# Kernel tuning notes

Measured on AMD Instinct MI355X. Metric: run time of the kernel, lower is better.

## Reference

```python
import jax, jax.numpy as jnp
import numpy as np

N = 50000       # nodes
E = 800000      # edges (avg degree 16)
IN_DIM = 64
H = 64          # hidden_dim
OUT_DIM = 64
R = 8           # n_relations
L = 3           # n_layers
LN_EPS = 1e-5
NEG_SLOPE = 0.2


def _layer_norm(x, g, b):
    mu = jnp.mean(x, axis=-1, keepdims=True)
    var = jnp.mean((x - mu) ** 2, axis=-1, keepdims=True)
    return (x - mu) * jax.lax.rsqrt(var + LN_EPS) * g + b


def setup_inputs() -> dict:
    key = jax.random.key(0)
    ks = jax.random.split(key, 10)
    s = 0.05
    return {
        "x": jax.random.normal(ks[0], (N, IN_DIM), jnp.float32),
        "edge_index": jax.random.randint(ks[1], (2, E), 0, N),
        "edge_type": jax.random.randint(ks[2], (E,), 0, R),
        "W_in": jax.random.normal(ks[3], (H, IN_DIM), jnp.float32) * s,
        "b_in": jnp.zeros((H,), jnp.float32),
        "W_rel": jax.random.normal(ks[4], (R, H, H), jnp.float32) * s,   # no bias
        "W_gate": jax.random.normal(ks[5], (R, H, H), jnp.float32) * s,
        "b_gate": jnp.zeros((R, H), jnp.float32),
        "W_att": jax.random.normal(ks[6], (R, 2 * H), jnp.float32) * s,  # Linear(2H,1) per relation
        "b_att": jnp.zeros((R,), jnp.float32),
        "ln_gamma": jnp.ones((L, H), jnp.float32),
        "ln_beta": jnp.zeros((L, H), jnp.float32),
        "W_out": jax.random.normal(ks[7], (OUT_DIM, H), jnp.float32) * s,
        "b_out": jnp.zeros((OUT_DIM,), jnp.float32),
    }


def reference(x, edge_index, edge_type, W_in, b_in, W_rel, W_gate, b_gate,
              W_att, b_att, ln_gamma, ln_beta, W_out, b_out):
    src, dst = edge_index[0], edge_index[1]
    Wa_src, Wa_dst = W_att[:, :H], W_att[:, H:]      # [R,H] each
    seg = dst * R + edge_type                        # combined (node, relation) scatter key
    eidx = jnp.arange(E)

    h = jax.nn.relu(x @ W_in.T + b_in)               # [N,H]

    for layer in range(L):
        h_src = h[src]                               # [E,H] gather
        h_dst = h[dst]                               # [E,H] gather
        # attention score of each edge under its own relation's Linear(2H,1)
        scores_all = h_src @ Wa_src.T + h_dst @ Wa_dst.T + b_att   # [E,R]
        scores = scores_all[eidx, edge_type]                        # [E]
        scores = jax.nn.leaky_relu(scores, NEG_SLOPE)
        # softmax over dim=0 within each relation's edge set (as in the torch code)
        m = jax.ops.segment_max(scores, edge_type, num_segments=R)
        ex = jnp.exp(scores - m[edge_type])
        denom = jax.ops.segment_sum(ex, edge_type, num_segments=R)
        att = ex / denom[edge_type]                                 # [E]
        # relation-specific linear of source features (linear commutes with gather)
        hWr = jnp.einsum('nh,rkh->nrk', h, W_rel)                   # [N,R,H]
        msg = hWr[src, edge_type] * att[:, None]                    # [E,H]
        # per-relation scatter-add into destinations
        agg = jax.ops.segment_sum(msg, seg, num_segments=N * R)     # [N*R,H]
        agg = agg.reshape(N, R, H)
        gate = jax.nn.sigmoid(jnp.einsum('nh,rkh->nrk', h, W_gate) + b_gate)  # [N,R,H]
        h_new = jnp.mean(gate * agg, axis=1)         # sum(messages)/n_relations
        h = jax.nn.relu(_layer_norm(h + h_new, ln_gamma[layer], ln_beta[layer]))

    return h @ W_out.T + b_out
```

## Files before the change

kernel.cpp:

```cpp
#include <hip/hip_runtime.h>
#include <math.h>

#define NN 50000
#define EE 800000
#define HH 64
#define RR 8
#define LL 3
#define NR (NN * RR)
#define NB ((NR + 255) / 256)
#define LN_EPS 1e-5f
#define NEG_SLOPE 0.2f
#define LDH 68
#define OTB (16 * LDH)
#define DSPREAD 64

typedef __attribute__((ext_vector_type(8))) short bf8;
typedef __attribute__((ext_vector_type(4))) float f4;
typedef __attribute__((ext_vector_type(2))) float f2;
typedef __attribute__((ext_vector_type(8))) unsigned short us8;
typedef __attribute__((ext_vector_type(2))) unsigned int u2;
typedef __attribute__((ext_vector_type(4))) unsigned int u4;

#define PIN(x) asm volatile("" :: "v"(x))

__device__ __forceinline__ unsigned short bf16r(float f) {
    unsigned u = __float_as_uint(f);
    unsigned r = u + 0x7fffu + ((u >> 16) & 1u);
    return (unsigned short)(r >> 16);
}
__device__ __forceinline__ float bf2f(unsigned short u) {
    return __uint_as_float(((unsigned)u) << 16);
}
__device__ __forceinline__ void stage16(const void* g, void* l) {
    __builtin_amdgcn_global_load_lds(
        (const __attribute__((address_space(1))) void*)g,
        (__attribute__((address_space(3))) void*)l, 16, 0, 0);
}

__global__ __launch_bounds__(256) void proj_in(
    const float* __restrict__ x, const float* __restrict__ W,
    const float* __restrict__ bias, const unsigned short* __restrict__ WaB,
    float* __restrict__ h, unsigned short* __restrict__ hbf,
    float* __restrict__ s_src, float* __restrict__ s_dst) {
    __shared__ float WT[64 * LDH];
    __shared__ float xs[16 * LDH];
    __shared__ float hs[16 * LDH];
    int tid = threadIdx.x;
    int n0 = blockIdx.x * 16;
    #pragma unroll
    for (int s = 0; s < 16; ++s) {
        int idx = tid + 256 * s;
        int k = idx >> 6, i = idx & 63;
        WT[i * LDH + k] = W[idx];
    }
    int row = tid >> 4, cg = tid & 15;
    {
        f4 v = ((const f4*)x)[(size_t)(n0 + row) * 16 + cg];
        *(f4*)&xs[row * LDH + cg * 4] = v;
    }
    __syncthreads();
    f4 acc;
    {
        f4 b = *(const f4*)(bias + cg * 4);
        acc = b;
        #pragma unroll
        for (int i = 0; i < 64; ++i) {
            float xv = xs[row * LDH + i];
            f4 wt = *(const f4*)&WT[i * LDH + cg * 4];
            acc[0] += xv * wt[0];
            acc[1] += xv * wt[1];
            acc[2] += xv * wt[2];
            acc[3] += xv * wt[3];
        }
        #pragma unroll
        for (int j = 0; j < 4; ++j) acc[j] = fmaxf(acc[j], 0.f);
        int n = n0 + row;
        *(f4*)(h + (size_t)n * 64 + cg * 4) = acc;
        u2 u;
        u[0] = (unsigned)bf16r(acc[0]) | ((unsigned)bf16r(acc[1]) << 16);
        u[1] = (unsigned)bf16r(acc[2]) | ((unsigned)bf16r(acc[3]) << 16);
        *(u2*)(hbf + (size_t)n * 64 + cg * 4) = u;
        *(f4*)&hs[row * LDH + cg * 4] = acc;
    }
    __syncthreads();
    if (tid < 64) {
        int lane = tid;
        int quad = lane >> 4, lr = lane & 15;
        f4 sc = (f4){0.f, 0.f, 0.f, 0.f};
        #pragma unroll
        for (int kb = 0; kb < 2; ++kb) {
            const float* p = &hs[lr * LDH + kb * 32 + quad * 8];
            bf8 a;
            #pragma unroll
            for (int j = 0; j < 8; ++j) a[j] = (short)bf16r(p[j]);
            const bf8* bw = (const bf8*)(WaB + lr * 64 + kb * 32 + quad * 8);
            sc = __builtin_amdgcn_mfma_f32_16x16x32_bf16(a, *bw, sc, 0, 0, 0);
        }
        #pragma unroll
        for (int j = 0; j < 4; ++j) {
            int n = n0 + quad * 4 + j;
            if (lr < 8) s_src[n * 8 + lr] = sc[j];
            else        s_dst[n * 8 + (lr - 8)] = sc[j];
        }
    }
}

__global__ void edge_count(const int* __restrict__ ei, const int* __restrict__ et,
                           int* __restrict__ counts, int* __restrict__ rank) {
    int e = blockIdx.x * 256 + threadIdx.x;
    int d = ei[EE + e], t = et[e];
    rank[e] = atomicAdd(&counts[d * 8 + t], 1);
}

__global__ void scan1(const int* __restrict__ counts, int* __restrict__ offs,
                      int* __restrict__ bsum) {
    __shared__ int s[256];
    int tid = threadIdx.x;
    int i = blockIdx.x * 256 + tid;
    int v = (i < NR) ? counts[i] : 0;
    s[tid] = v; __syncthreads();
    for (int d = 1; d < 256; d <<= 1) {
        int x = (tid >= d) ? s[tid - d] : 0;
        __syncthreads();
        s[tid] += x;
        __syncthreads();
    }
    if (i < NR) offs[i] = s[tid] - v;
    if (tid == 255) bsum[blockIdx.x] = s[255];
}

__global__ void scan2(int* __restrict__ bsum) {
    __shared__ int s[1024];
    int tid = threadIdx.x;
    int carry = 0;
    for (int c0 = 0; c0 < NB; c0 += 1024) {
        int i = c0 + tid;
        int v = (i < NB) ? bsum[i] : 0;
        s[tid] = v; __syncthreads();
        for (int d = 1; d < 1024; d <<= 1) {
            int x = (tid >= d) ? s[tid - d] : 0;
            __syncthreads();
            s[tid] += x;
            __syncthreads();
        }
        if (i < NB) bsum[i] = carry + s[tid] - v;
        int tot = s[1023];
        __syncthreads();
        carry += tot;
    }
}

__global__ void edge_fill(const int* __restrict__ ei, const int* __restrict__ et,
                          const int* __restrict__ rank, const int* __restrict__ offs,
                          const int* __restrict__ bsum, u2* __restrict__ spack) {
    int e = blockIdx.x * 256 + threadIdx.x;
    int s = ei[e], d = ei[EE + e], t = et[e];
    int seg = d * 8 + t;
    int slot = offs[seg] + bsum[seg >> 8] + rank[e];
    spack[slot] = (u2){(unsigned)s, (unsigned)seg};
}

__global__ void cvt_w(const float* __restrict__ Wr, const float* __restrict__ Wg,
                      const float* __restrict__ Wa, const float* __restrict__ Wo,
                      unsigned short* __restrict__ WrB, unsigned short* __restrict__ WgB,
                      unsigned short* __restrict__ WaB, unsigned short* __restrict__ WoB) {
    int i = blockIdx.x * 256 + threadIdx.x;
    WrB[i] = bf16r(Wr[i]);
    WgB[i] = bf16r(Wg[i]);
    if (i < 1024) {
        int row = i >> 6, k = i & 63;
        float v = (row < 8) ? Wa[row * 128 + k] : Wa[(row - 8) * 128 + 64 + k];
        WaB[i] = bf16r(v);
    }
    if (i < 4096) WoB[i] = bf16r(Wo[i]);
}

__global__ void edge_softmax2(const u2* __restrict__ spack,
                              const float* __restrict__ s_src, const float* __restrict__ s_dst,
                              const float* __restrict__ b_att,
                              u2* __restrict__ epack, float* __restrict__ dpart) {
    __shared__ float lsum[4][8];
    int tid = threadIdx.x;
    if (tid < 32) lsum[tid >> 3][tid & 7] = 0.f;
    __syncthreads();
    int slot = blockIdx.x * 256 + tid;
    u2 sp = spack[slot];
    int src = (int)sp[0];
    int seg = (int)sp[1];
    int t = seg & 7;
    float sc = s_src[src * 8 + t] + s_dst[seg] + b_att[t];
    sc = (sc >= 0.f) ? sc : NEG_SLOPE * sc;
    float ex = __expf(sc);
    epack[slot] = (u2){(unsigned)src, __float_as_uint(ex)};
    atomicAdd(&lsum[tid >> 6][t], ex);
    __syncthreads();
    if (tid < 8) {
        float v = lsum[0][tid] + lsum[1][tid] + lsum[2][tid] + lsum[3][tid];
        atomicAdd(&dpart[(blockIdx.x & (DSPREAD - 1)) * 16 + tid], v);
    }
}

__global__ void denom_reduce(const float* __restrict__ dpartL,
                             float* __restrict__ idn8L) {
    __shared__ float sb[256];
    int t = threadIdx.x;
    int rb = t >> 3, ty = t & 7;
    float v = dpartL[rb * 16 + ty] + dpartL[(rb + 32) * 16 + ty];
    sb[t] = v; __syncthreads();
    for (int st = 128; st >= 8; st >>= 1) {
        if (t < st) sb[t] += sb[t + st];
        __syncthreads();
    }
    if (t < 8) idn8L[t] = 1.f / sb[t];
}

__global__ __launch_bounds__(256, 4) void gather_seg(
    const int* __restrict__ offs, const int* __restrict__ bsum,
    const u2* __restrict__ epack, const float* __restrict__ idn8L,
    const unsigned short* __restrict__ hbf_in,
    unsigned short* __restrict__ psG) {
    int tid = threadIdx.x;
    int segl = tid >> 1, half = tid & 1;
    int sidx = blockIdx.x * 128 + segl;
    int lo = offs[sidx] + bsum[sidx >> 8];
    int nxt = sidx + 1;
    int hi = (nxt < NR) ? (offs[nxt] + bsum[nxt >> 8]) : EE;
    int r = segl & 7, gn = segl >> 3;

    f4 d0 = *(const f4*)(idn8L);
    f4 d1 = *(const f4*)(idn8L + 4);
    float i01 = (r & 1) ? d0[1] : d0[0];
    float i23 = (r & 1) ? d0[3] : d0[2];
    float i45 = (r & 1) ? d1[1] : d1[0];
    float i67 = (r & 1) ? d1[3] : d1[2];
    float i03 = (r & 2) ? i23 : i01;
    float i47 = (r & 2) ? i67 : i45;
    float idn = (r & 4) ? i47 : i03;

    f2 acc[16];
    #pragma unroll
    for (int i = 0; i < 16; ++i) acc[i] = (f2){0.f, 0.f};

    for (int s = lo; s < hi; s += 4) {
        int i1 = (s + 1 < hi) ? s + 1 : s;
        int i2 = (s + 2 < hi) ? s + 2 : s;
        int i3 = (s + 3 < hi) ? s + 3 : s;
        u2 pk0 = epack[s], pk1 = epack[i1], pk2 = epack[i2], pk3 = epack[i3];
        float a0 = __uint_as_float(pk0[1]);
        float a1 = (s + 1 < hi) ? __uint_as_float(pk1[1]) : 0.f;
        float a2 = (s + 2 < hi) ? __uint_as_float(pk2[1]) : 0.f;
        float a3 = (s + 3 < hi) ? __uint_as_float(pk3[1]) : 0.f;
        const u4* hp0 = (const u4*)(hbf_in + ((size_t)(int)pk0[0] << 6) + half * 32);
        const u4* hp1 = (const u4*)(hbf_in + ((size_t)(int)pk1[0] << 6) + half * 32);
        const u4* hp2 = (const u4*)(hbf_in + ((size_t)(int)pk2[0] << 6) + half * 32);
        const u4* hp3 = (const u4*)(hbf_in + ((size_t)(int)pk3[0] << 6) + half * 32);
        #pragma unroll
        for (int q = 0; q < 4; ++q) {
            u4 v0 = hp0[q], v1 = hp1[q], v2 = hp2[q], v3 = hp3[q];
            #pragma unroll
            for (int k = 0; k < 4; ++k) {
                f2 w0, w1, w2, w3;
                w0[0] = __uint_as_float(v0[k] << 16);
                w0[1] = __uint_as_float(v0[k] & 0xffff0000u);
                w1[0] = __uint_as_float(v1[k] << 16);
                w1[1] = __uint_as_float(v1[k] & 0xffff0000u);
                w2[0] = __uint_as_float(v2[k] << 16);
                w2[1] = __uint_as_float(v2[k] & 0xffff0000u);
                w3[0] = __uint_as_float(v3[k] << 16);
                w3[1] = __uint_as_float(v3[k] & 0xffff0000u);
                acc[q * 4 + k] += (f2){a0, a0} * w0;
                acc[q * 4 + k] += (f2){a1, a1} * w1;
                acc[q * 4 + k] += (f2){a2, a2} * w2;
                acc[q * 4 + k] += (f2){a3, a3} * w3;
            }
        }
    }

    unsigned short* base = psG + ((size_t)blockIdx.x << 13) + gn * 512 + r * 64;
    #pragma unroll
    for (int q = 0; q < 4; ++q) {
        us8 o;
        #pragma unroll
        for (int k = 0; k < 4; ++k) {
            o[2 * k]     = bf16r(acc[q * 4 + k][0] * idn);
            o[2 * k + 1] = bf16r(acc[q * 4 + k][1] * idn);
        }
        int c2 = (half * 4 + q) ^ (gn & 7);
        *(us8*)(base + c2 * 8) = o;
    }
}

template<bool EMIT, bool OUT>
__global__ __launch_bounds__(256, 2) void combine_dense(
    const float* __restrict__ hbuf, const unsigned short* __restrict__ psG,
    const unsigned short* __restrict__ WrB, const unsigned short* __restrict__ WgB,
    const unsigned short* __restrict__ WaB, const unsigned short* __restrict__ WoB,
    const float* __restrict__ b_gate, const float* __restrict__ gamma,
    const float* __restrict__ beta, float* __restrict__ hout,
    unsigned short* __restrict__ hbf_out, float* __restrict__ ssrc_out,
    float* __restrict__ sdst_out, float* __restrict__ outp,
    const float* __restrict__ b_out) {
    __shared__ unsigned short psL[8192];
    __shared__ float hsL[1024];
    __shared__ float tf[32 * LDH];
    int tid = threadIdx.x;
    int n0 = blockIdx.x * 16;
    int w = tid >> 6, lane = tid & 63;
    int quad = lane >> 4, lr = lane & 15;
    int tn = w;

    {
        const char* pslice = (const char*)psG + ((size_t)blockIdx.x << 14);
        #pragma unroll
        for (int i = 0; i < 4; ++i) {
            unsigned off = i * 4096 + w * 1024;
            stage16(pslice + off + lane * 16, (char*)psL + off);
        }
        unsigned a = w * 1024 + lane * 16;
        unsigned sa = a ^ (((a >> 8) & 7u) << 4);
        stage16((const char*)(hbuf + (size_t)n0 * 64) + sa, (char*)hsL + a);
    }

    bf8 wfr[8][2], wfg[8][2];
    #pragma unroll
    for (int r = 0; r < 8; ++r) {
        #pragma unroll
        for (int kb = 0; kb < 2; ++kb) {
            wfr[r][kb] = *(const bf8*)(WrB + r * 4096 + (tn * 16 + lr) * 64 + kb * 32 + quad * 8);
            wfg[r][kb] = *(const bf8*)(WgB + r * 4096 + (tn * 16 + lr) * 64 + kb * 32 + quad * 8);
        }
    }
    float bgv[8];
    #pragma unroll
    for (int r = 0; r < 8; ++r) bgv[r] = b_gate[r * 64 + tn * 16 + lr];
    f4 gmv = *(const f4*)(gamma + (tid & 15) * 4);
    f4 btv = *(const f4*)(beta + (tid & 15) * 4);
    bf8 wa0, wa1, wo0, wo1;
    float bo = 0.f;
    if (EMIT) {
        wa0 = *(const bf8*)(WaB + lr * 64 + 0 * 32 + quad * 8);
        wa1 = *(const bf8*)(WaB + lr * 64 + 1 * 32 + quad * 8);
    }
    if (OUT) {
        wo0 = *(const bf8*)(WoB + (tn * 16 + lr) * 64 + 0 * 32 + quad * 8);
        wo1 = *(const bf8*)(WoB + (tn * 16 + lr) * 64 + 1 * 32 + quad * 8);
        bo = b_out[tn * 16 + lr];
    }
    #pragma unroll
    for (int r = 0; r < 8; ++r) {
        PIN(wfr[r][0]); PIN(wfr[r][1]);
        PIN(wfg[r][0]); PIN(wfg[r][1]);
        PIN(bgv[r]);
    }
    PIN(gmv); PIN(btv);
    if (EMIT) { PIN(wa0); PIN(wa1); }
    if (OUT)  { PIN(wo0); PIN(wo1); PIN(bo); }

    __syncthreads();

    bf8 a_h[2];
    #pragma unroll
    for (int kb = 0; kb < 2; ++kb) {
        unsigned c0 = (unsigned)(kb * 8 + quad * 2)     ^ (unsigned)(lr & 7);
        unsigned c1 = (unsigned)(kb * 8 + quad * 2 + 1) ^ (unsigned)(lr & 7);
        f4 p0 = *(const f4*)((const char*)hsL + lr * 256 + c0 * 16);
        f4 p1 = *(const f4*)((const char*)hsL + lr * 256 + c1 * 16);
        bf8 a;
        #pragma unroll
        for (int j = 0; j < 4; ++j) a[j] = (short)bf16r(p0[j]);
        #pragma unroll
        for (int j = 0; j < 4; ++j) a[4 + j] = (short)bf16r(p1[j]);
        a_h[kb] = a;
    }

    f4 acc = (f4){0.f, 0.f, 0.f, 0.f};
    #pragma unroll
    for (int r = 0; r < 8; ++r) {
        bf8 a_p[2];
        #pragma unroll
        for (int kb = 0; kb < 2; ++kb) {
            unsigned c = (unsigned)(kb * 4 + quad) ^ (unsigned)(lr & 7);
            a_p[kb] = *(const bf8*)((const char*)psL + lr * 1024 + r * 128 + c * 16);
        }
        f4 aggc = (f4){0.f, 0.f, 0.f, 0.f};
        f4 gacc = (f4){0.f, 0.f, 0.f, 0.f};
        #pragma unroll
        for (int kb = 0; kb < 2; ++kb) {
            aggc = __builtin_amdgcn_mfma_f32_16x16x32_bf16(a_p[kb], wfr[r][kb], aggc, 0, 0, 0);
            gacc = __builtin_amdgcn_mfma_f32_16x16x32_bf16(a_h[kb], wfg[r][kb], gacc, 0, 0, 0);
        }
        #pragma unroll
        for (int j = 0; j < 4; ++j) {
            float g = 1.f / (1.f + __expf(-(gacc[j] + bgv[r])));
            acc[j] += g * aggc[j];
        }
    }

    #pragma unroll
    for (int j = 0; j < 4; ++j) {
        int row = quad * 4 + j;
        int col = tn * 16 + lr;
        unsigned y = (unsigned)(row * 256 + col * 4);
        float hres = *(const float*)((const char*)hsL + (y ^ (((unsigned)(row & 7)) << 4)));
        tf[row * LDH + col] = hres + acc[j] * 0.125f;
    }
    __syncthreads();

    {
        int row = tid >> 4, c = tid & 15;
        int n = n0 + row;
        f4 tv = *(const f4*)&tf[row * LDH + c * 4];
        float s1 = tv[0] + tv[1] + tv[2] + tv[3];
        float s2 = tv[0]*tv[0] + tv[1]*tv[1] + tv[2]*tv[2] + tv[3]*tv[3];
        #pragma unroll
        for (int off = 1; off <= 8; off <<= 1) {
            s1 += __shfl_xor(s1, off, 64);
            s2 += __shfl_xor(s2, off, 64);
        }
        float mu = s1 * (1.f / 64.f);
        float var = s2 * (1.f / 64.f) - mu * mu;
        float rs = rsqrtf(var + LN_EPS);
        f4 ov;
        #pragma unroll
        for (int j = 0; j < 4; ++j)
            ov[j] = fmaxf((tv[j] - mu) * rs * gmv[j] + btv[j], 0.f);
        if (!OUT)
            *(f4*)(hout + (size_t)n * 64 + c * 4) = ov;
        *(f4*)&tf[OTB + row * LDH + c * 4] = ov;
        if (EMIT) {
            u2 u;
            u[0] = (unsigned)bf16r(ov[0]) | ((unsigned)bf16r(ov[1]) << 16);
            u[1] = (unsigned)bf16r(ov[2]) | ((unsigned)bf16r(ov[3]) << 16);
            *(u2*)(hbf_out + (size_t)n * 64 + c * 4) = u;
        }
    }

    if (EMIT) {
        __syncthreads();
        if (w == 0) {
            f4 sc = (f4){0.f, 0.f, 0.f, 0.f};
            #pragma unroll
            for (int kb = 0; kb < 2; ++kb) {
                const float* p = &tf[OTB + lr * LDH + kb * 32 + quad * 8];
                bf8 a;
                #pragma unroll
                for (int j = 0; j < 8; ++j) a[j] = (short)bf16r(p[j]);
                sc = __builtin_amdgcn_mfma_f32_16x16x32_bf16(a, kb ? wa1 : wa0, sc, 0, 0, 0);
            }
            #pragma unroll
            for (int j = 0; j < 4; ++j) {
                int n = n0 + quad * 4 + j;
                if (lr < 8) ssrc_out[n * 8 + lr] = sc[j];
                else        sdst_out[n * 8 + (lr - 8)] = sc[j];
            }
        }
    }

    if (OUT) {
        __syncthreads();
        f4 oc = (f4){0.f, 0.f, 0.f, 0.f};
        #pragma unroll
        for (int kb = 0; kb < 2; ++kb) {
            const float* p = &tf[OTB + lr * LDH + kb * 32 + quad * 8];
            bf8 a;
            #pragma unroll
            for (int j = 0; j < 8; ++j) a[j] = (short)bf16r(p[j]);
            oc = __builtin_amdgcn_mfma_f32_16x16x32_bf16(a, kb ? wo1 : wo0, oc, 0, 0, 0);
        }
        #pragma unroll
        for (int j = 0; j < 4; ++j)
            outp[(size_t)(n0 + quad * 4 + j) * 64 + tn * 16 + lr] = oc[j] + bo;
    }
}

extern "C" void kernel_launch(void* const* d_in, const int* in_sizes, int n_in,
                              void* d_out, int out_size, void* d_ws, size_t ws_size,
                              hipStream_t stream) {
    const float* x      = (const float*)d_in[0];
    const int*   ei     = (const int*)d_in[1];
    const int*   et     = (const int*)d_in[2];
    const float* W_in   = (const float*)d_in[3];
    const float* b_in   = (const float*)d_in[4];
    const float* W_rel  = (const float*)d_in[5];
    const float* W_gate = (const float*)d_in[6];
    const float* b_gate = (const float*)d_in[7];
    const float* W_att  = (const float*)d_in[8];
    const float* b_att  = (const float*)d_in[9];
    const float* ln_g   = (const float*)d_in[10];
    const float* ln_b   = (const float*)d_in[11];
    const float* W_out  = (const float*)d_in[12];
    const float* b_out  = (const float*)d_in[13];
    float* out = (float*)d_out;

    float* h0 = (float*)d_out;

    char* ws = (char*)d_ws;
    float* h1 = (float*)ws;                     ws += (size_t)NN * 64 * 4;
    unsigned short* hbfA = (unsigned short*)ws; ws += (size_t)NN * 64 * 2;
    unsigned short* hbfB = (unsigned short*)ws; ws += (size_t)NN * 64 * 2;
    float* s_src = (float*)ws;                  ws += (size_t)NN * 8 * 4;
    float* s_dst = (float*)ws;                  ws += (size_t)NN * 8 * 4;
    unsigned short* WrB = (unsigned short*)ws;  ws += (size_t)RR * 64 * 64 * 2;
    unsigned short* WgB = (unsigned short*)ws;  ws += (size_t)RR * 64 * 64 * 2;
    unsigned short* WaB = (unsigned short*)ws;  ws += 2048;
    unsigned short* WoB = (unsigned short*)ws;  ws += 8192;
    int* counts = (int*)ws;                     ws += (size_t)NR * 4;
    float* dpart = (float*)ws;                  ws += 3 * DSPREAD * 16 * 4;
    float* idn8G = (float*)ws;                  ws += 3 * 16 * 4;
    int* offs = (int*)ws;                       ws += (size_t)NR * 4;
    int* bsum = (int*)ws;                       ws += 6400;
    int* rank = (int*)ws;                       ws += (size_t)EE * 4;
    u2* spack = (u2*)ws;                        ws += (size_t)EE * 8;
    u2* epack = (u2*)ws;                        ws += (size_t)EE * 8;
    unsigned short* psG = (unsigned short*)ws;  ws += (size_t)NR * 64 * 2;

    hipMemsetAsync(counts, 0, (size_t)NR * 4 + 3 * DSPREAD * 16 * 4, stream);
    cvt_w<<<128, 256, 0, stream>>>(W_rel, W_gate, W_att, W_out, WrB, WgB, WaB, WoB);
    edge_count<<<EE / 256, 256, 0, stream>>>(ei, et, counts, rank);
    scan1<<<NB, 256, 0, stream>>>(counts, offs, bsum);
    scan2<<<1, 1024, 0, stream>>>(bsum);
    edge_fill<<<EE / 256, 256, 0, stream>>>(ei, et, rank, offs, bsum, spack);
    proj_in<<<NN / 16, 256, 0, stream>>>(x, W_in, b_in, WaB, h0, hbfA, s_src, s_dst);

    const int tiles16 = NN / 16;
    float* hA = h0;  float* hB = h1;
    unsigned short* bfA = hbfA;  unsigned short* bfB = hbfB;
    for (int layer = 0; layer < LL; ++layer) {
        float* dpl = dpart + (size_t)layer * DSPREAD * 16;
        float* idn = idn8G + (size_t)layer * 16;
        edge_softmax2<<<EE / 256, 256, 0, stream>>>(spack, s_src, s_dst, b_att,
                                                    epack, dpl);
        denom_reduce<<<1, 256, 0, stream>>>(dpl, idn);
        gather_seg<<<tiles16, 256, 0, stream>>>(offs, bsum, epack, idn, bfA, psG);
        if (layer < LL - 1) {
            combine_dense<true, false><<<tiles16, 256, 0, stream>>>(
                hA, psG, WrB, WgB, WaB, WoB, b_gate,
                ln_g + layer * 64, ln_b + layer * 64,
                hB, bfB, s_src, s_dst, out, b_out);
        } else {
            combine_dense<false, true><<<tiles16, 256, 0, stream>>>(
                hA, psG, WrB, WgB, WaB, WoB, b_gate,
                ln_g + layer * 64, ln_b + layer * 64,
                hB, bfB, s_src, s_dst, out, b_out);
        }
        float* tf = hA; hA = hB; hB = tf;
        unsigned short* tb = bfA; bfA = bfB; bfB = tb;
    }
}
```

Baseline: 466.2 us.

## Stream relation weights through a triple-buffered register pipeline and raise occupancy

```diff
diff --git a/kernel.cpp b/kernel.cpp
--- a/kernel.cpp
+++ b/kernel.cpp
@@ -23,6 +23,15 @@
 
 #define PIN(x) asm volatile("" :: "v"(x))
 
+#define WLOADP(d0, d1, sbase, vbyte) \
+    asm volatile("global_load_dwordx4 %0, %2, %3 offset:0\n\t" \
+                 "global_load_dwordx4 %1, %2, %3 offset:64" \
+        : "=&v"(d0), "=&v"(d1) : "v"(vbyte), "s"(sbase) : "memory")
+#define WWAIT4() do { asm volatile("s_waitcnt vmcnt(4)" ::: "memory"); \
+    __builtin_amdgcn_sched_barrier(0); } while (0)
+#define WWAIT0() do { asm volatile("s_waitcnt vmcnt(0)" ::: "memory"); \
+    __builtin_amdgcn_sched_barrier(0); } while (0)
+
 __device__ __forceinline__ unsigned short bf16r(float f) {
     unsigned u = __float_as_uint(f);
     unsigned r = u + 0x7fffu + ((u >> 16) & 1u);
@@ -30,6 +39,9 @@
 }
 __device__ __forceinline__ float bf2f(unsigned short u) {
     return __uint_as_float(((unsigned)u) << 16);
+}
+__device__ __forceinline__ bf8 asbf8(u4 v) {
+    union { u4 a; bf8 b; } c; c.a = v; return c.b;
 }
 __device__ __forceinline__ void stage16(const void* g, void* l) {
     __builtin_amdgcn_global_load_lds(
@@ -291,7 +303,7 @@
 }
 
 template<bool EMIT, bool OUT>
-__global__ __launch_bounds__(256, 2) void combine_dense(
+__global__ __launch_bounds__(256, 4) void combine_dense(
     const float* __restrict__ hbuf, const unsigned short* __restrict__ psG,
     const unsigned short* __restrict__ WrB, const unsigned short* __restrict__ WgB,
     const unsigned short* __restrict__ WaB, const unsigned short* __restrict__ WoB,
@@ -302,7 +314,7 @@
     const float* __restrict__ b_out) {
     __shared__ unsigned short psL[8192];
     __shared__ float hsL[1024];
-    __shared__ float tf[32 * LDH];
+    float* ps_f = (float*)psL;
     int tid = threadIdx.x;
     int n0 = blockIdx.x * 16;
     int w = tid >> 6, lane = tid & 63;
@@ -320,43 +332,20 @@
         unsigned sa = a ^ (((a >> 8) & 7u) << 4);
         stage16((const char*)(hbuf + (size_t)n0 * 64) + sa, (char*)hsL + a);
     }
-
-    bf8 wfr[8][2], wfg[8][2];
-    #pragma unroll
-    for (int r = 0; r < 8; ++r) {
-        #pragma unroll
-        for (int kb = 0; kb < 2; ++kb) {
-            wfr[r][kb] = *(const bf8*)(WrB + r * 4096 + (tn * 16 + lr) * 64 + kb * 32 + quad * 8);
-            wfg[r][kb] = *(const bf8*)(WgB + r * 4096 + (tn * 16 + lr) * 64 + kb * 32 + quad * 8);
-        }
-    }
     float bgv[8];
     #pragma unroll
     for (int r = 0; r < 8; ++r) bgv[r] = b_gate[r * 64 + tn * 16 + lr];
-    f4 gmv = *(const f4*)(gamma + (tid & 15) * 4);
-    f4 btv = *(const f4*)(beta + (tid & 15) * 4);
-    bf8 wa0, wa1, wo0, wo1;
-    float bo = 0.f;
-    if (EMIT) {
-        wa0 = *(const bf8*)(WaB + lr * 64 + 0 * 32 + quad * 8);
-        wa1 = *(const bf8*)(WaB + lr * 64 + 1 * 32 + quad * 8);
-    }
-    if (OUT) {
-        wo0 = *(const bf8*)(WoB + (tn * 16 + lr) * 64 + 0 * 32 + quad * 8);
-        wo1 = *(const bf8*)(WoB + (tn * 16 + lr) * 64 + 1 * 32 + quad * 8);
-        bo = b_out[tn * 16 + lr];
-    }
-    #pragma unroll
-    for (int r = 0; r < 8; ++r) {
-        PIN(wfr[r][0]); PIN(wfr[r][1]);
-        PIN(wfg[r][0]); PIN(wfg[r][1]);
-        PIN(bgv[r]);
-    }
-    PIN(gmv); PIN(btv);
-    if (EMIT) { PIN(wa0); PIN(wa1); }
-    if (OUT)  { PIN(wo0); PIN(wo1); PIN(bo); }
-
-    __syncthreads();
+    #pragma unroll
+    for (int r = 0; r < 8; ++r) PIN(bgv[r]);
+
+    __syncthreads();
+
+    unsigned rowb = (unsigned)((tn * 16 + lr) * 128 + quad * 16);
+    u4 wr[3][2], wg[3][2];
+    WLOADP(wr[0][0], wr[0][1], WrB, rowb);
+    WLOADP(wg[0][0], wg[0][1], WgB, rowb);
+    WLOADP(wr[1][0], wr[1][1], WrB, rowb + 8192u);
+    WLOADP(wg[1][0], wg[1][1], WgB, rowb + 8192u);
 
     bf8 a_h[2];
     #pragma unroll
@@ -376,18 +365,25 @@
     f4 acc = (f4){0.f, 0.f, 0.f, 0.f};
     #pragma unroll
     for (int r = 0; r < 8; ++r) {
+        if (r < 7) { WWAIT4(); } else { WWAIT0(); }
         bf8 a_p[2];
         #pragma unroll
         for (int kb = 0; kb < 2; ++kb) {
             unsigned c = (unsigned)(kb * 4 + quad) ^ (unsigned)(lr & 7);
             a_p[kb] = *(const bf8*)((const char*)psL + lr * 1024 + r * 128 + c * 16);
         }
+        int rb = r % 3;
         f4 aggc = (f4){0.f, 0.f, 0.f, 0.f};
         f4 gacc = (f4){0.f, 0.f, 0.f, 0.f};
-        #pragma unroll
-        for (int kb = 0; kb < 2; ++kb) {
-            aggc = __builtin_amdgcn_mfma_f32_16x16x32_bf16(a_p[kb], wfr[r][kb], aggc, 0, 0, 0);
-            gacc = __builtin_amdgcn_mfma_f32_16x16x32_bf16(a_h[kb], wfg[r][kb], gacc, 0, 0, 0);
+        aggc = __builtin_amdgcn_mfma_f32_16x16x32_bf16(a_p[0], asbf8(wr[rb][0]), aggc, 0, 0, 0);
+        gacc = __builtin_amdgcn_mfma_f32_16x16x32_bf16(a_h[0], asbf8(wg[rb][0]), gacc, 0, 0, 0);
+        aggc = __builtin_amdgcn_mfma_f32_16x16x32_bf16(a_p[1], asbf8(wr[rb][1]), aggc, 0, 0, 0);
+        gacc = __builtin_amdgcn_mfma_f32_16x16x32_bf16(a_h[1], asbf8(wg[rb][1]), gacc, 0, 0, 0);
+        if (r + 2 < 8) {
+            int nb = (r + 2) % 3;
+            unsigned vo = rowb + (unsigned)(r + 2) * 8192u;
+            WLOADP(wr[nb][0], wr[nb][1], WrB, vo);
+            WLOADP(wg[nb][0], wg[nb][1], WgB, vo);
         }
         #pragma unroll
         for (int j = 0; j < 4; ++j) {
@@ -395,6 +391,7 @@
             acc[j] += g * aggc[j];
         }
     }
+    __syncthreads();
 
     #pragma unroll
     for (int j = 0; j < 4; ++j) {
@@ -402,14 +399,14 @@
         int col = tn * 16 + lr;
         unsigned y = (unsigned)(row * 256 + col * 4);
         float hres = *(const float*)((const char*)hsL + (y ^ (((unsigned)(row & 7)) << 4)));
-        tf[row * LDH + col] = hres + acc[j] * 0.125f;
+        ps_f[row * LDH + col] = hres + acc[j] * 0.125f;
     }
     __syncthreads();
 
     {
         int row = tid >> 4, c = tid & 15;
         int n = n0 + row;
-        f4 tv = *(const f4*)&tf[row * LDH + c * 4];
+        f4 tv = *(const f4*)&ps_f[row * LDH + c * 4];
         float s1 = tv[0] + tv[1] + tv[2] + tv[3];
         float s2 = tv[0]*tv[0] + tv[1]*tv[1] + tv[2]*tv[2] + tv[3]*tv[3];
         #pragma unroll
@@ -420,13 +417,15 @@
         float mu = s1 * (1.f / 64.f);
         float var = s2 * (1.f / 64.f) - mu * mu;
         float rs = rsqrtf(var + LN_EPS);
+        f4 g = *(const f4*)(gamma + c * 4);
+        f4 b = *(const f4*)(beta + c * 4);
         f4 ov;
         #pragma unroll
         for (int j = 0; j < 4; ++j)
-            ov[j] = fmaxf((tv[j] - mu) * rs * gmv[j] + btv[j], 0.f);
+            ov[j] = fmaxf((tv[j] - mu) * rs * g[j] + b[j], 0.f);
         if (!OUT)
             *(f4*)(hout + (size_t)n * 64 + c * 4) = ov;
-        *(f4*)&tf[OTB + row * LDH + c * 4] = ov;
+        *(f4*)&ps_f[OTB + row * LDH + c * 4] = ov;
         if (EMIT) {
             u2 u;
             u[0] = (unsigned)bf16r(ov[0]) | ((unsigned)bf16r(ov[1]) << 16);
@@ -441,11 +440,12 @@
             f4 sc = (f4){0.f, 0.f, 0.f, 0.f};
             #pragma unroll
             for (int kb = 0; kb < 2; ++kb) {
-                const float* p = &tf[OTB + lr * LDH + kb * 32 + quad * 8];
+                const float* p = &ps_f[OTB + lr * LDH + kb * 32 + quad * 8];
                 bf8 a;
                 #pragma unroll
                 for (int j = 0; j < 8; ++j) a[j] = (short)bf16r(p[j]);
-                sc = __builtin_amdgcn_mfma_f32_16x16x32_bf16(a, kb ? wa1 : wa0, sc, 0, 0, 0);
+                const bf8* bw = (const bf8*)(WaB + lr * 64 + kb * 32 + quad * 8);
+                sc = __builtin_amdgcn_mfma_f32_16x16x32_bf16(a, *bw, sc, 0, 0, 0);
             }
             #pragma unroll
             for (int j = 0; j < 4; ++j) {
@@ -461,12 +461,14 @@
         f4 oc = (f4){0.f, 0.f, 0.f, 0.f};
         #pragma unroll
         for (int kb = 0; kb < 2; ++kb) {
-            const float* p = &tf[OTB + lr * LDH + kb * 32 + quad * 8];
+            const float* p = &ps_f[OTB + lr * LDH + kb * 32 + quad * 8];
             bf8 a;
             #pragma unroll
             for (int j = 0; j < 8; ++j) a[j] = (short)bf16r(p[j]);
-            oc = __builtin_amdgcn_mfma_f32_16x16x32_bf16(a, kb ? wo1 : wo0, oc, 0, 0, 0);
-        }
+            const bf8* bw = (const bf8*)(WoB + ((tn * 16 + lr) * 64 + kb * 32 + quad * 8));
+            oc = __builtin_amdgcn_mfma_f32_16x16x32_bf16(a, *bw, oc, 0, 0, 0);
+        }
+        float bo = b_out[tn * 16 + lr];
         #pragma unroll
         for (int j = 0; j < 4; ++j)
             outp[(size_t)(n0 + quad * 4 + j) * 64 + tn * 16 + lr] = oc[j] + bo;
```

Result: no change. 460.1 us (-1.3%).
